# Kernel optimization log

Measured on AMD Instinct MI355X. Metric: run time of the kernel, lower is better.

## Reference

```python
import jax, jax.numpy as jnp
import numpy as np

D_MODEL = 2048
NUM_HEADS = 32
NUM_KV_HEADS = 8
DIM_HEAD = D_MODEL // NUM_HEADS  # 64
REPS = NUM_HEADS // NUM_KV_HEADS  # 4
B, T = 2, 2048


def setup_inputs() -> dict:
    key = jax.random.key(0)
    k_x, k_q, k_k, k_v, k_o = jax.random.split(key, 5)
    s = 1.0 / np.sqrt(D_MODEL)
    return {
        "x": jax.random.normal(k_x, (B, T, D_MODEL), dtype=jnp.float32),
        "wq": jax.random.normal(k_q, (D_MODEL, NUM_HEADS * DIM_HEAD), dtype=jnp.float32) * s,
        "wk": jax.random.normal(k_k, (D_MODEL, NUM_KV_HEADS * DIM_HEAD), dtype=jnp.float32) * s,
        "wv": jax.random.normal(k_v, (D_MODEL, NUM_KV_HEADS * DIM_HEAD), dtype=jnp.float32) * s,
        "wo": jax.random.normal(k_o, (D_MODEL, D_MODEL), dtype=jnp.float32) * s,
    }


def reference(x, wq, wk, wv, wo):
    Bb, Tt, _ = x.shape
    q = (x @ wq).reshape(Bb, Tt, NUM_HEADS, DIM_HEAD)       # [B,T,H,dh]
    k = (x @ wk).reshape(Bb, Tt, NUM_KV_HEADS, DIM_HEAD)    # [B,T,Hkv,dh]
    v = (x @ wv).reshape(Bb, Tt, NUM_KV_HEADS, DIM_HEAD)
    # repeat_interleave KV heads to match Q heads
    k = jnp.repeat(k, REPS, axis=2)                          # [B,T,H,dh]
    v = jnp.repeat(v, REPS, axis=2)
    scale = 1.0 / np.sqrt(DIM_HEAD).astype(np.float32)
    scores = jnp.einsum('bqhd,bkhd->bhqk', q, k) * scale     # [B,H,T,T]
    causal = jnp.tril(jnp.ones((Tt, Tt), dtype=bool))
    scores = jnp.where(causal, scores, -jnp.inf)
    attn = jax.nn.softmax(scores, axis=-1)
    out = jnp.einsum('bhqk,bkhd->bqhd', attn, v)             # [B,T,H,dh]
    out = out.reshape(Bb, Tt, NUM_HEADS * DIM_HEAD)
    return out @ wo
```

## Files before the change

### kernel.cpp

```cpp
#include <hip/hip_runtime.h>

typedef unsigned short u16;
typedef unsigned int u32;
typedef unsigned long long u64;

typedef __bf16 bf16x8 __attribute__((ext_vector_type(8)));
typedef float f32x4 __attribute__((ext_vector_type(4)));
typedef u16 u16x4 __attribute__((ext_vector_type(4)));

__device__ __forceinline__ u16 f2bf(float f) {
  u32 u = __builtin_bit_cast(u32, f);
  u += 0x7fffu + ((u >> 16) & 1u);
  return (u16)(u >> 16);
}

__device__ __forceinline__ u32 packbf2(float a, float b) {
  __bf16 x = (__bf16)a, y = (__bf16)b;
  return (u32)__builtin_bit_cast(u16, x) | ((u32)__builtin_bit_cast(u16, y) << 16);
}

__device__ __forceinline__ float fexp2(float x) {
#if __has_builtin(__builtin_amdgcn_exp2f)
  return __builtin_amdgcn_exp2f(x);
#else
  return exp2f(x);
#endif
}

__device__ __forceinline__ void gload_lds16(const void* g, void* lds) {
  __builtin_amdgcn_global_load_lds(
      (const __attribute__((address_space(1))) void*)g,
      (__attribute__((address_space(3))) void*)lds, 16, 0, 0);
}

#define QSCALE 0.18033688011112043f

__global__ __launch_bounds__(256) void prep_kernel(
    const float* __restrict__ x, u16* __restrict__ xb,
    const float* __restrict__ wq, const float* __restrict__ wk,
    const float* __restrict__ wv, const float* __restrict__ wo,
    u16* __restrict__ wqT, u16* __restrict__ wkT,
    u16* __restrict__ wvT, u16* __restrict__ woT) {
  __shared__ float tile[32][33];
  int bid = blockIdx.x;
  if (bid < 8192) {
    int i = (bid * 256 + threadIdx.x) * 4;
    float4 v = *reinterpret_cast<const float4*>(x + i);
    u16x4 o;
    o[0] = f2bf(v.x); o[1] = f2bf(v.y); o[2] = f2bf(v.z); o[3] = f2bf(v.w);
    *reinterpret_cast<u16x4*>(xb + i) = o;
    return;
  }
  bid -= 8192;
  constexpr int K = 2048;
  const float* w_;
  u16* wt;
  int N;
  switch (bid >> 12) {
    case 0: w_ = wq; wt = wqT; N = 2048; break;
    case 1: w_ = wo; wt = woT; N = 2048; break;
    case 2: w_ = wk; wt = wkT; N = 512; break;
    default: w_ = wv; wt = wvT; N = 512; break;
  }
  int rem = bid & 4095;
  int bx = (rem & 63) * 32;
  if (bx >= N) return;
  int by = (rem >> 6) * 32;
  int tx = threadIdx.x & 31, ty = threadIdx.x >> 5;
#pragma unroll
  for (int i = 0; i < 32; i += 8)
    tile[ty + i][tx] = w_[(size_t)(by + ty + i) * N + bx + tx];
  __syncthreads();
#pragma unroll
  for (int i = 0; i < 32; i += 8)
    wt[(size_t)(bx + ty + i) * K + by + tx] = f2bf(tile[tx][ty + i]);
}

__global__ __launch_bounds__(512, 1) void gemm_qkv(
    const u16* __restrict__ A, const u16* __restrict__ BT,
    u16* __restrict__ Cb, u16* __restrict__ Cb2, u16* __restrict__ Cb3) {
  constexpr int K = 2048, NT = 32;
  __shared__ __align__(16) u16 Ab[2][256 * 64];
  __shared__ __align__(16) u16 Bb[2][192 * 64];
  const int t = threadIdx.x;
  const int lane = t & 63;
  const int w = t >> 6;
  const int wm = w >> 2, wn = w & 3;
  const int l15 = lane & 15, l4 = lane >> 4;

  const int nwg = gridDim.x * gridDim.y;
  const int bid = blockIdx.y * gridDim.x + blockIdx.x;
  const int wg = (bid & 7) * (nwg >> 3) + (bid >> 3);
  const int brow = (wg / gridDim.x) * 256;
  const int bcol = (wg % gridDim.x) * 192;

  const int r0 = t >> 3;
  const int gc = ((t & 7) ^ (r0 & 7)) * 8;
  auto stageA = [&](int q, int h, int kt) {
    const u16* src = A + (size_t)(brow + h * 128 + r0) * K + kt * 64 + gc;
    u16* dst = &Ab[q][(h * 128 + r0) * 64 + (t & 7) * 8];
    gload_lds16(src, dst);
    gload_lds16(src + (size_t)64 * K, dst + 64 * 64);
  };
  auto stageB = [&](int q, int c, int kt) {
    const u16* src = BT + (size_t)(bcol + c * 64 + r0) * K + kt * 64 + gc;
    u16* dst = &Bb[q][(c * 64 + r0) * 64 + (t & 7) * 8];
    gload_lds16(src, dst);
  };

  f32x4 acc[8][3];
#pragma unroll
  for (int mi = 0; mi < 8; mi++)
#pragma unroll
    for (int n = 0; n < 3; n++)
#pragma unroll
      for (int r = 0; r < 4; r++) acc[mi][n][r] = 0.f;

  stageA(0, 0, 0); stageA(0, 1, 0);
  stageB(0, 0, 0); stageB(0, 1, 0); stageB(0, 2, 0);
  stageA(1, 0, 1); stageA(1, 1, 1);
  asm volatile("s_waitcnt vmcnt(4)" ::: "memory");
  __builtin_amdgcn_sched_barrier(0);
  __builtin_amdgcn_s_barrier();

  for (int kt = 0; kt < NT; ++kt) {
    const int q = kt & 1;
    const u16* Al = Ab[q];
    const u16* Bl = Bb[q];
    bf16x8 af[8][2], bf[3][2];

#pragma unroll
    for (int m = 0; m < 4; ++m) {
      int row = wm * 128 + m * 16 + l15;
#pragma unroll
      for (int ks = 0; ks < 2; ++ks)
        af[m][ks] = *reinterpret_cast<const bf16x8*>(
            &Al[row * 64 + (((ks * 4 + l4) ^ (row & 7)) * 8)]);
    }
#pragma unroll
    for (int n = 0; n < 3; ++n) {
      int row = wn * 48 + n * 16 + l15;
#pragma unroll
      for (int ks = 0; ks < 2; ++ks)
        bf[n][ks] = *reinterpret_cast<const bf16x8*>(
            &Bl[row * 64 + (((ks * 4 + l4) ^ (row & 7)) * 8)]);
    }
    if (kt + 1 < NT) stageB(q ^ 1, 0, kt + 1);
    __builtin_amdgcn_s_barrier();
    __builtin_amdgcn_s_setprio(1);
#pragma unroll
    for (int ks = 0; ks < 2; ++ks)
#pragma unroll
      for (int m = 0; m < 4; ++m)
#pragma unroll
        for (int n = 0; n < 2; ++n)
          acc[m][n] = __builtin_amdgcn_mfma_f32_16x16x32_bf16(
              af[m][ks], bf[n][ks], acc[m][n], 0, 0, 0);
    __builtin_amdgcn_s_setprio(0);
    __builtin_amdgcn_s_barrier();

#pragma unroll
    for (int m = 4; m < 8; ++m) {
      int row = wm * 128 + m * 16 + l15;
#pragma unroll
      for (int ks = 0; ks < 2; ++ks)
        af[m][ks] = *reinterpret_cast<const bf16x8*>(
            &Al[row * 64 + (((ks * 4 + l4) ^ (row & 7)) * 8)]);
    }
    if (kt + 1 < NT) { stageB(q ^ 1, 1, kt + 1); stageB(q ^ 1, 2, kt + 1); }
    __builtin_amdgcn_s_barrier();
    __builtin_amdgcn_s_setprio(1);
#pragma unroll
    for (int ks = 0; ks < 2; ++ks)
#pragma unroll
      for (int m = 0; m < 4; ++m)
        acc[m][2] = __builtin_amdgcn_mfma_f32_16x16x32_bf16(
            af[m][ks], bf[2][ks], acc[m][2], 0, 0, 0);
    __builtin_amdgcn_s_setprio(0);
    __builtin_amdgcn_s_barrier();

    if (kt + 2 < NT) stageA(q, 0, kt + 2);
    __builtin_amdgcn_s_barrier();
    __builtin_amdgcn_s_setprio(1);
#pragma unroll
    for (int ks = 0; ks < 2; ++ks)
#pragma unroll
      for (int m = 4; m < 8; ++m)
#pragma unroll
        for (int n = 0; n < 2; ++n)
          acc[m][n] = __builtin_amdgcn_mfma_f32_16x16x32_bf16(
              af[m][ks], bf[n][ks], acc[m][n], 0, 0, 0);
    __builtin_amdgcn_s_setprio(0);
    __builtin_amdgcn_s_barrier();

    if (kt + 2 < NT) stageA(q, 1, kt + 2);
    __builtin_amdgcn_s_barrier();
    __builtin_amdgcn_s_setprio(1);
#pragma unroll
    for (int ks = 0; ks < 2; ++ks)
#pragma unroll
      for (int m = 4; m < 8; ++m)
        acc[m][2] = __builtin_amdgcn_mfma_f32_16x16x32_bf16(
            af[m][ks], bf[2][ks], acc[m][2], 0, 0, 0);
    __builtin_amdgcn_s_setprio(0);
    if (kt + 2 < NT) {
      asm volatile("s_waitcnt vmcnt(4)" ::: "memory");
    } else {
      asm volatile("s_waitcnt vmcnt(0)" ::: "memory");
    }
    __builtin_amdgcn_sched_barrier(0);
    __builtin_amdgcn_s_barrier();
  }

#pragma unroll
  for (int mi = 0; mi < 8; ++mi) {
    int grow0 = brow + wm * 128 + mi * 16 + l4 * 4;
#pragma unroll
    for (int n = 0; n < 3; ++n) {
      int gbase = bcol + wn * 48 + n * 16;
      int gcol = gbase + l15;
      if (gbase < 2048) {
#pragma unroll
        for (int r = 0; r < 4; ++r)
          Cb[(size_t)(grow0 + r) * 2048 + gcol] = f2bf(acc[mi][n][r] * QSCALE);
      } else if (gbase < 2560) {
#pragma unroll
        for (int r = 0; r < 4; ++r)
          Cb2[(size_t)(grow0 + r) * 512 + (gcol - 2048)] = f2bf(acc[mi][n][r]);
      } else {
        int col = gcol - 2560;
        int bb = grow0 >> 11, tt = grow0 & 2047;
        u64 wv = (u64)packbf2(acc[mi][n][0], acc[mi][n][1]) |
                 ((u64)packbf2(acc[mi][n][2], acc[mi][n][3]) << 32);
        *reinterpret_cast<u64*>(&Cb3[((size_t)(bb * 512 + col)) * 2048 + tt]) = wv;
      }
    }
  }
}

__global__ __launch_bounds__(512, 2) void gemm256n(
    const u16* __restrict__ A, const u16* __restrict__ BT,
    float* __restrict__ Cf, int M, int N) {
  constexpr int K = 2048, NT = 32;
  __shared__ __align__(16) u16 Ab[2][256 * 64];
  __shared__ __align__(16) u16 Bb[2][128 * 64];
  const int t = threadIdx.x;
  const int lane = t & 63;
  const int w = t >> 6;
  const int wm = w >> 1, wn = w & 1;
  const int l15 = lane & 15, l4 = lane >> 4;

  const int nwg = gridDim.x * gridDim.y;
  const int bid = blockIdx.y * gridDim.x + blockIdx.x;
  const int wg = (bid & 7) * (nwg >> 3) + (bid >> 3);
  const int brow = (wg / gridDim.x) * 256;
  const int bcol = (wg % gridDim.x) * 128;

  const int r0 = t >> 3;
  const int gc = ((t & 7) ^ (r0 & 7)) * 8;
  auto stageA = [&](int q, int h, int kt) {
    const u16* src = A + (size_t)(brow + h * 128 + r0) * K + kt * 64 + gc;
    u16* dst = &Ab[q][(h * 128 + r0) * 64 + (t & 7) * 8];
    gload_lds16(src, dst);
    gload_lds16(src + (size_t)64 * K, dst + 64 * 64);
  };
  auto stageB = [&](int q, int h, int kt) {
    const u16* src = BT + (size_t)(bcol + h * 64 + r0) * K + kt * 64 + gc;
    u16* dst = &Bb[q][(h * 64 + r0) * 64 + (t & 7) * 8];
    gload_lds16(src, dst);
  };

  f32x4 acc[4][4];
#pragma unroll
  for (int m = 0; m < 4; m++)
#pragma unroll
    for (int n = 0; n < 4; n++)
#pragma unroll
      for (int r = 0; r < 4; r++) acc[m][n][r] = 0.f;

  stageA(0, 0, 0); stageA(0, 1, 0);
  stageB(0, 0, 0); stageB(0, 1, 0);
  stageA(1, 0, 1); stageA(1, 1, 1);
  asm volatile("s_waitcnt vmcnt(4)" ::: "memory");
  __builtin_amdgcn_sched_barrier(0);
  __builtin_amdgcn_s_barrier();

  for (int kt = 0; kt < NT; ++kt) {
    const int q = kt & 1;
    const u16* Al = Ab[q];
    const u16* Bl = Bb[q];
    bf16x8 af[4][2], bf[4][2];

#pragma unroll
    for (int m = 0; m < 2; ++m) {
      int row = wm * 64 + m * 16 + l15;
#pragma unroll
      for (int ks = 0; ks < 2; ++ks)
        af[m][ks] = *reinterpret_cast<const bf16x8*>(
            &Al[row * 64 + (((ks * 4 + l4) ^ (row & 7)) * 8)]);
    }
#pragma unroll
    for (int n = 0; n < 2; ++n) {
      int row = wn * 64 + n * 16 + l15;
#pragma unroll
      for (int ks = 0; ks < 2; ++ks)
        bf[n][ks] = *reinterpret_cast<const bf16x8*>(
            &Bl[row * 64 + (((ks * 4 + l4) ^ (row & 7)) * 8)]);
    }
    if (kt + 1 < NT) stageB(q ^ 1, 0, kt + 1);
    __builtin_amdgcn_s_barrier();
    __builtin_amdgcn_s_setprio(1);
#pragma unroll
    for (int ks = 0; ks < 2; ++ks)
#pragma unroll
      for (int m = 0; m < 2; ++m)
#pragma unroll
        for (int n = 0; n < 2; ++n)
          acc[m][n] = __builtin_amdgcn_mfma_f32_16x16x32_bf16(
              af[m][ks], bf[n][ks], acc[m][n], 0, 0, 0);
    __builtin_amdgcn_s_setprio(0);
    __builtin_amdgcn_s_barrier();

#pragma unroll
    for (int m = 2; m < 4; ++m) {
      int row = wm * 64 + m * 16 + l15;
#pragma unroll
      for (int ks = 0; ks < 2; ++ks)
        af[m][ks] = *reinterpret_cast<const bf16x8*>(
            &Al[row * 64 + (((ks * 4 + l4) ^ (row & 7)) * 8)]);
    }
#pragma unroll
    for (int n = 2; n < 4; ++n) {
      int row = wn * 64 + n * 16 + l15;
#pragma unroll
      for (int ks = 0; ks < 2; ++ks)
        bf[n][ks] = *reinterpret_cast<const bf16x8*>(
            &Bl[row * 64 + (((ks * 4 + l4) ^ (row & 7)) * 8)]);
    }
    if (kt + 1 < NT) stageB(q ^ 1, 1, kt + 1);
    __builtin_amdgcn_s_barrier();
    __builtin_amdgcn_s_setprio(1);
#pragma unroll
    for (int ks = 0; ks < 2; ++ks)
#pragma unroll
      for (int m = 0; m < 2; ++m)
#pragma unroll
        for (int n = 2; n < 4; ++n)
          acc[m][n] = __builtin_amdgcn_mfma_f32_16x16x32_bf16(
              af[m][ks], bf[n][ks], acc[m][n], 0, 0, 0);
    __builtin_amdgcn_s_setprio(0);
    __builtin_amdgcn_s_barrier();

    if (kt + 2 < NT) stageA(q, 0, kt + 2);
    __builtin_amdgcn_s_barrier();
    __builtin_amdgcn_s_setprio(1);
#pragma unroll
    for (int ks = 0; ks < 2; ++ks)
#pragma unroll
      for (int m = 2; m < 4; ++m)
#pragma unroll
        for (int n = 0; n < 2; ++n)
          acc[m][n] = __builtin_amdgcn_mfma_f32_16x16x32_bf16(
              af[m][ks], bf[n][ks], acc[m][n], 0, 0, 0);
    __builtin_amdgcn_s_setprio(0);
    __builtin_amdgcn_s_barrier();

    if (kt + 2 < NT) stageA(q, 1, kt + 2);
    __builtin_amdgcn_s_barrier();
    __builtin_amdgcn_s_setprio(1);
#pragma unroll
    for (int ks = 0; ks < 2; ++ks)
#pragma unroll
      for (int m = 2; m < 4; ++m)
#pragma unroll
        for (int n = 2; n < 4; ++n)
          acc[m][n] = __builtin_amdgcn_mfma_f32_16x16x32_bf16(
              af[m][ks], bf[n][ks], acc[m][n], 0, 0, 0);
    __builtin_amdgcn_s_setprio(0);
    if (kt + 2 < NT) {
      asm volatile("s_waitcnt vmcnt(4)" ::: "memory");
    } else {
      asm volatile("s_waitcnt vmcnt(0)" ::: "memory");
    }
    __builtin_amdgcn_sched_barrier(0);
    __builtin_amdgcn_s_barrier();
  }

#pragma unroll
  for (int m = 0; m < 4; ++m) {
    int grow0 = brow + wm * 64 + m * 16 + l4 * 4;
#pragma unroll
    for (int n = 0; n < 4; ++n) {
      int gcol = bcol + wn * 64 + n * 16 + l15;
#pragma unroll
      for (int r = 0; r < 4; ++r)
        Cf[(size_t)(grow0 + r) * N + gcol] = acc[m][n][r];
    }
  }
}

__global__ __launch_bounds__(256, 4) void attn_kernel(
    const u16* __restrict__ Qb, const u16* __restrict__ Kb,
    const u16* __restrict__ VT, u16* __restrict__ Ob) {
  const int bx = blockIdx.x;
  const int kvh = bx & 7;
  const int u = bx >> 3;
  const int jj = u & 15;
  const int v = u >> 4;
  const int h = kvh * 4 + (v & 3);
  const int b = v >> 2;
  const int t = threadIdx.x;
  const int lane = t & 63;
  const int w = t >> 6;
  const int q15 = lane & 15, g = lane >> 4;

  __shared__ __align__(16) u16 Ks[2][64 * 64];
  __shared__ __align__(16) u16 Vs[2][64 * 64];
  __shared__ __align__(16) u32 Pu[4][16 * 32];

  const size_t Krow0 = (size_t)b * 2048;
  const size_t Vrow0 = ((size_t)b * 8 + kvh) * 64;

  u16* const dk0 = &Ks[0][t * 8];
  u16* const dk1 = &Ks[1][t * 8];
  u16* const dv0 = &Vs[0][t * 8];
  u16* const dv1 = &Vs[1][t * 8];
  const int row0 = t >> 3;
  const int gcs = ((t & 7) ^ (row0 & 7)) * 8;
  const u16* const pk0 = Kb + (Krow0 + row0) * 512 + kvh * 64 + gcs;
  const u16* const pv0 = VT + (Vrow0 + row0) * 2048 + gcs;
  const u16* kp = pk0;
  const u16* vp = pv0;

  auto stage = [&](int buf, const u16* kpp, const u16* vpp) {
    u16* dk = buf ? dk1 : dk0;
    u16* dv = buf ? dv1 : dv0;
    gload_lds16(kpp, dk);
    gload_lds16(kpp + 32 * 512, dk + 2048);
    gload_lds16(vpp, dv);
    gload_lds16(vpp + 32 * 2048, dv + 2048);
  };

  const int swzB = (q15 & 7) << 3;
  const int swzP = (q15 & 7) << 2;
  u32* const pw = &Pu[w][0];
  const int nA = 32 - jj;
  const int nsteps = 33;

  stage(0, kp, vp);
  __syncthreads();
  int cur = 0;
  int ss = 0;

#pragma unroll
  for (int ph = 0; ph < 2; ++ph) {
    const int qt = ph ? jj : 31 - jj;
    const int nkv = qt + 1;
    const int wq0 = qt * 64 + w * 16;

    bf16x8 qf[2];
    {
      const u16* q0 = &Qb[((size_t)b * 2048 + wq0 + q15) * 2048 + h * 64 + g * 8];
      qf[0] = *reinterpret_cast<const bf16x8*>(q0);
      qf[1] = *reinterpret_cast<const bf16x8*>(q0 + 32);
    }

    f32x4 oo[4];
#pragma unroll
    for (int c = 0; c < 4; c++)
#pragma unroll
      for (int r = 0; r < 4; r++) oo[c][r] = 0.f;
    float mr = -1e30f, lr = 0.f;

    for (int kv = 0; kv < nkv; ++kv, ++ss) {
      const int kvbase = kv << 6;
      if (ss + 1 < nsteps) {
        if (ss + 1 == nA) {
          kp = pk0;
          vp = pv0;
        } else {
          kp += 64 * 512;
          vp += 64;
        }
        stage(cur ^ 1, kp, vp);
      }

      f32x4 s[4];
#pragma unroll
      for (int c = 0; c < 4; c++)
#pragma unroll
        for (int r = 0; r < 4; r++) s[c][r] = 0.f;
      __builtin_amdgcn_s_setprio(1);
#pragma unroll
      for (int ks = 0; ks < 2; ++ks) {
        const int kcol = (ks * 32 + g * 8) ^ swzB;
#pragma unroll
        for (int c = 0; c < 4; c++) {
          bf16x8 kb = *reinterpret_cast<const bf16x8*>(
              &Ks[cur][(c * 16 + q15) * 64 + kcol]);
          s[c] = __builtin_amdgcn_mfma_f32_16x16x32_bf16(kb, qf[ks], s[c], 0, 0, 0);
        }
      }
      __builtin_amdgcn_s_setprio(0);

      if (kv == qt) {
        const int qg = wq0 + q15;
#pragma unroll
        for (int c = 0; c < 4; c++)
#pragma unroll
          for (int r = 0; r < 4; r++)
            if (kvbase + c * 16 + g * 4 + r > qg) s[c][r] = -1e30f;
      }

      float mx0 = fmaxf(fmaxf(s[0][0], s[0][1]), fmaxf(s[0][2], s[0][3]));
      float mx1 = fmaxf(fmaxf(s[1][0], s[1][1]), fmaxf(s[1][2], s[1][3]));
      float mx2 = fmaxf(fmaxf(s[2][0], s[2][1]), fmaxf(s[2][2], s[2][3]));
      float mx3 = fmaxf(fmaxf(s[3][0], s[3][1]), fmaxf(s[3][2], s[3][3]));
      float mx = fmaxf(fmaxf(mx0, mx1), fmaxf(mx2, mx3));
      mx = fmaxf(mx, __shfl_xor(mx, 16));
      mx = fmaxf(mx, __shfl_xor(mx, 32));
      if (!__all(mx <= mr + 8.f)) {
        float mnew = fmaxf(mr, mx);
        float alpha = fexp2(mr - mnew);
        lr *= alpha;
#pragma unroll
        for (int c = 0; c < 4; c++)
#pragma unroll
          for (int r = 0; r < 4; r++) oo[c][r] *= alpha;
        mr = mnew;
      }
      float p[4][4];
      float rs = 0.f;
#pragma unroll
      for (int c = 0; c < 4; c++) {
        float t0 = fexp2(s[c][0] - mr);
        float t1 = fexp2(s[c][1] - mr);
        float t2 = fexp2(s[c][2] - mr);
        float t3 = fexp2(s[c][3] - mr);
        p[c][0] = t0; p[c][1] = t1; p[c][2] = t2; p[c][3] = t3;
        rs += (t0 + t1) + (t2 + t3);
      }
      rs += __shfl_xor(rs, 16);
      rs += __shfl_xor(rs, 32);
      lr += rs;
#pragma unroll
      for (int c = 0; c < 4; c++) {
        u64 wv = (u64)packbf2(p[c][0], p[c][1]) |
                 ((u64)packbf2(p[c][2], p[c][3]) << 32);
        *reinterpret_cast<u64*>(&pw[q15 * 32 + ((c * 8 + g * 2) ^ swzP)]) = wv;
      }
      bf16x8 pb[2];
#pragma unroll
      for (int ks = 0; ks < 2; ++ks)
        pb[ks] = *reinterpret_cast<const bf16x8*>(
            &pw[q15 * 32 + ((ks * 16 + g * 4) ^ swzP)]);

      __builtin_amdgcn_s_setprio(1);
#pragma unroll
      for (int ks = 0; ks < 2; ++ks) {
        const int vcol = (ks * 32 + g * 8) ^ swzB;
#pragma unroll
        for (int c2 = 0; c2 < 4; c2++) {
          bf16x8 vb = *reinterpret_cast<const bf16x8*>(
              &Vs[cur][(c2 * 16 + q15) * 64 + vcol]);
          oo[c2] = __builtin_amdgcn_mfma_f32_16x16x32_bf16(vb, pb[ks], oo[c2], 0, 0, 0);
        }
      }
      __builtin_amdgcn_s_setprio(0);

      __syncthreads();
      cur ^= 1;
    }

    const int qq = lane >> 2, cl = lane & 3;
    const int swq = (qq & 7) << 2;
    {
      float rcp = 1.0f / lr;
#pragma unroll
      for (int c2 = 0; c2 < 4; c2++) {
        u64 wv = (u64)packbf2(oo[c2][0] * rcp, oo[c2][1] * rcp) |
                 ((u64)packbf2(oo[c2][2] * rcp, oo[c2][3] * rcp) << 32);
        *reinterpret_cast<u64*>(&pw[q15 * 32 + ((c2 * 8 + g * 2) ^ swzP)]) = wv;
      }
      uint4 d0 = *reinterpret_cast<const uint4*>(&pw[qq * 32 + ((cl * 4) ^ swq)]);
      uint4 d1 = *reinterpret_cast<const uint4*>(&pw[qq * 32 + ((cl * 4 + 16) ^ swq)]);
      u32* og = (u32*)Ob + ((size_t)b * 2048 + wq0 + qq) * 1024 + h * 32;
      *reinterpret_cast<uint4*>(&og[cl * 4]) = d0;
      *reinterpret_cast<uint4*>(&og[cl * 4 + 16]) = d1;
    }
  }
}

extern "C" void kernel_launch(void* const* d_in, const int* in_sizes, int n_in,
                              void* d_out, int out_size, void* d_ws, size_t ws_size,
                              hipStream_t stream) {
  const float* x = (const float*)d_in[0];
  const float* wq = (const float*)d_in[1];
  const float* wk = (const float*)d_in[2];
  const float* wv = (const float*)d_in[3];
  const float* wo = (const float*)d_in[4];
  float* out = (float*)d_out;

  char* p = (char*)d_ws;
  u16* xb = (u16*)p;   p += (size_t)4096 * 2048 * 2;
  u16* wqT = (u16*)p;  p += (size_t)2048 * 2048 * 2;
  u16* wkT = (u16*)p;  p += (size_t)512 * 2048 * 2;
  u16* wvT = (u16*)p;  p += (size_t)512 * 2048 * 2;
  u16* woT = (u16*)p;  p += (size_t)2048 * 2048 * 2;
  u16* Qb = (u16*)p;   p += (size_t)4096 * 2048 * 2;
  u16* Kb = (u16*)p;   p += (size_t)4096 * 512 * 2;
  u16* VTb = (u16*)p;  p += (size_t)2 * 512 * 2048 * 2;
  u16* attn = xb;

  prep_kernel<<<8192 + 16384, 256, 0, stream>>>(
      x, xb, wq, wk, wv, wo, wqT, wkT, wvT, woT);

  gemm_qkv<<<dim3(16, 16), 512, 0, stream>>>(xb, wqT, Qb, Kb, VTb);

  attn_kernel<<<1024, 256, 0, stream>>>(Qb, Kb, VTb, attn);

  gemm256n<<<dim3(2048 / 128, 4096 / 256), 512, 0, stream>>>(
      attn, woT, out, 4096, 2048);
}
```

Before: 185.1 us.

## Use 32x32 MFMA with 128-row query tiles in attention, keep P in registers

The attention kernel moves from 64-row to 128-row query tiles, with each wave owning 32 query rows. QK^T and PV now use 32x32x16 bf16 MFMAs, halving the grid to 512 blocks with launch bounds lowered to 2. The P matrix is rearranged between lanes with cross-half shuffles instead of an LDS round-trip, and waves skip KV tiles that lie wholly beyond their causal limit. This aims to reuse each staged K/V tile across more queries and cut LDS traffic, at the cost of more registers, lower occupancy, fewer blocks and some idle waves on diagonal tiles.

```diff
diff --git a/kernel.cpp b/kernel.cpp
--- a/kernel.cpp
+++ b/kernel.cpp
@@ -6,7 +6,9 @@
 
 typedef __bf16 bf16x8 __attribute__((ext_vector_type(8)));
 typedef float f32x4 __attribute__((ext_vector_type(4)));
+typedef float f32x16 __attribute__((ext_vector_type(16)));
 typedef u16 u16x4 __attribute__((ext_vector_type(4)));
+typedef u32 u32x4v __attribute__((ext_vector_type(4)));
 
 __device__ __forceinline__ u16 f2bf(float f) {
   u32 u = __builtin_bit_cast(u32, f);
@@ -399,24 +401,25 @@
   }
 }
 
-__global__ __launch_bounds__(256, 4) void attn_kernel(
+__global__ __launch_bounds__(256, 2) void attn_kernel(
     const u16* __restrict__ Qb, const u16* __restrict__ Kb,
     const u16* __restrict__ VT, u16* __restrict__ Ob) {
   const int bx = blockIdx.x;
   const int kvh = bx & 7;
   const int u = bx >> 3;
-  const int jj = u & 15;
-  const int v = u >> 4;
+  const int jj = u & 7;
+  const int v = u >> 3;
   const int h = kvh * 4 + (v & 3);
   const int b = v >> 2;
   const int t = threadIdx.x;
   const int lane = t & 63;
   const int w = t >> 6;
-  const int q15 = lane & 15, g = lane >> 4;
+  const int q31 = lane & 31;
+  const int hi = lane >> 5;
 
   __shared__ __align__(16) u16 Ks[2][64 * 64];
   __shared__ __align__(16) u16 Vs[2][64 * 64];
-  __shared__ __align__(16) u32 Pu[4][16 * 32];
+  __shared__ __align__(16) u32 Po[4][32 * 32];
 
   const size_t Krow0 = (size_t)b * 2048;
   const size_t Vrow0 = ((size_t)b * 8 + kvh) * 64;
@@ -441,11 +444,9 @@
     gload_lds16(vpp + 32 * 2048, dv + 2048);
   };
 
-  const int swzB = (q15 & 7) << 3;
-  const int swzP = (q15 & 7) << 2;
-  u32* const pw = &Pu[w][0];
-  const int nA = 32 - jj;
-  const int nsteps = 33;
+  const int swk = (q31 & 7);
+  const int nA = 2 * (15 - jj) + 2;
+  const int nsteps = 34;
 
   stage(0, kp, vp);
   __syncthreads();
@@ -454,22 +455,23 @@
 
 #pragma unroll
   for (int ph = 0; ph < 2; ++ph) {
-    const int qt = ph ? jj : 31 - jj;
-    const int nkv = qt + 1;
-    const int wq0 = qt * 64 + w * 16;
-
-    bf16x8 qf[2];
+    const int qt = ph ? jj : 15 - jj;
+    const int nkv = 2 * qt + 2;
+    const int wq0 = qt * 128 + w * 32;
+    const int mylast = (wq0 + 31) >> 6;
+
+    bf16x8 qf[4];
     {
-      const u16* q0 = &Qb[((size_t)b * 2048 + wq0 + q15) * 2048 + h * 64 + g * 8];
+      const u16* q0 = &Qb[((size_t)b * 2048 + wq0 + q31) * 2048 + h * 64 + hi * 8];
       qf[0] = *reinterpret_cast<const bf16x8*>(q0);
-      qf[1] = *reinterpret_cast<const bf16x8*>(q0 + 32);
-    }
-
-    f32x4 oo[4];
-#pragma unroll
-    for (int c = 0; c < 4; c++)
-#pragma unroll
-      for (int r = 0; r < 4; r++) oo[c][r] = 0.f;
+      qf[1] = *reinterpret_cast<const bf16x8*>(q0 + 16);
+      qf[2] = *reinterpret_cast<const bf16x8*>(q0 + 32);
+      qf[3] = *reinterpret_cast<const bf16x8*>(q0 + 48);
+    }
+
+    f32x16 oo0, oo1;
+#pragma unroll
+    for (int r = 0; r < 16; ++r) { oo0[r] = 0.f; oo1[r] = 0.f; }
     float mr = -1e30f, lr = 0.f;
 
     for (int kv = 0; kv < nkv; ++kv, ++ss) {
@@ -485,109 +487,138 @@
         stage(cur ^ 1, kp, vp);
       }
 
-      f32x4 s[4];
-#pragma unroll
-      for (int c = 0; c < 4; c++)
-#pragma unroll
-        for (int r = 0; r < 4; r++) s[c][r] = 0.f;
-      __builtin_amdgcn_s_setprio(1);
-#pragma unroll
-      for (int ks = 0; ks < 2; ++ks) {
-        const int kcol = (ks * 32 + g * 8) ^ swzB;
-#pragma unroll
-        for (int c = 0; c < 4; c++) {
-          bf16x8 kb = *reinterpret_cast<const bf16x8*>(
-              &Ks[cur][(c * 16 + q15) * 64 + kcol]);
-          s[c] = __builtin_amdgcn_mfma_f32_16x16x32_bf16(kb, qf[ks], s[c], 0, 0, 0);
+      if (kv <= mylast) {
+        f32x16 s0, s1;
+#pragma unroll
+        for (int r = 0; r < 16; ++r) { s0[r] = 0.f; s1[r] = 0.f; }
+        __builtin_amdgcn_s_setprio(1);
+#pragma unroll
+        for (int kc = 0; kc < 4; ++kc) {
+          const int kcol = ((kc * 2 + hi) ^ swk) * 8;
+          bf16x8 kb0 = *reinterpret_cast<const bf16x8*>(&Ks[cur][q31 * 64 + kcol]);
+          bf16x8 kb1 = *reinterpret_cast<const bf16x8*>(&Ks[cur][(32 + q31) * 64 + kcol]);
+          s0 = __builtin_amdgcn_mfma_f32_32x32x16_bf16(kb0, qf[kc], s0, 0, 0, 0);
+          s1 = __builtin_amdgcn_mfma_f32_32x32x16_bf16(kb1, qf[kc], s1, 0, 0, 0);
         }
+        __builtin_amdgcn_s_setprio(0);
+
+        if (kvbase + 63 > wq0) {
+          const int qg = wq0 + q31;
+#pragma unroll
+          for (int r = 0; r < 16; ++r) {
+            int crow = ((r >> 2) << 3) + (r & 3) + 4 * hi;
+            if (kvbase + crow > qg) s0[r] = -1e30f;
+            if (kvbase + 32 + crow > qg) s1[r] = -1e30f;
+          }
+        }
+
+        float mt[8];
+#pragma unroll
+        for (int r = 0; r < 8; ++r)
+          mt[r] = fmaxf(fmaxf(s0[r], s0[r + 8]), fmaxf(s1[r], s1[r + 8]));
+#pragma unroll
+        for (int st = 4; st; st >>= 1)
+#pragma unroll
+          for (int r = 0; r < 8; ++r)
+            if (r < st) mt[r] = fmaxf(mt[r], mt[r + st]);
+        float mx = fmaxf(mt[0], __shfl_xor(mt[0], 32));
+        if (!__all(mx <= mr + 8.f)) {
+          float mnew = fmaxf(mr, mx);
+          float alpha = fexp2(mr - mnew);
+          lr *= alpha;
+#pragma unroll
+          for (int r = 0; r < 16; ++r) { oo0[r] *= alpha; oo1[r] *= alpha; }
+          mr = mnew;
+        }
+        float st_[8];
+#pragma unroll
+        for (int r = 0; r < 16; ++r) {
+          s0[r] = fexp2(s0[r] - mr);
+          s1[r] = fexp2(s1[r] - mr);
+        }
+#pragma unroll
+        for (int r = 0; r < 8; ++r)
+          st_[r] = (s0[r] + s0[r + 8]) + (s1[r] + s1[r + 8]);
+#pragma unroll
+        for (int stp = 4; stp; stp >>= 1)
+#pragma unroll
+          for (int r = 0; r < 8; ++r)
+            if (r < stp) st_[r] += st_[r + stp];
+        float rs = st_[0] + __shfl_xor(st_[0], 32);
+        lr += rs;
+
+        u32 W0[4][2], W1[4][2];
+#pragma unroll
+        for (int rr = 0; rr < 4; ++rr)
+#pragma unroll
+          for (int sx = 0; sx < 2; ++sx) {
+            W0[rr][sx] = packbf2(s0[4 * rr + 2 * sx], s0[4 * rr + 2 * sx + 1]);
+            W1[rr][sx] = packbf2(s1[4 * rr + 2 * sx], s1[4 * rr + 2 * sx + 1]);
+          }
+        bf16x8 pb[4];
+#pragma unroll
+        for (int cc = 0; cc < 2; ++cc) {
+          const int rrA = 2 * cc, rrB = 2 * cc + 1;
+          {
+            u32 z0 = hi ? W0[rrA][0] : W0[rrB][0];
+            u32 z1 = hi ? W0[rrA][1] : W0[rrB][1];
+            u32 z0x = (u32)__shfl_xor((int)z0, 32);
+            u32 z1x = (u32)__shfl_xor((int)z1, 32);
+            u32x4v pv4 = {hi ? z0x : W0[rrA][0], hi ? z1x : W0[rrA][1],
+                          hi ? W0[rrB][0] : z0x, hi ? W0[rrB][1] : z1x};
+            pb[cc] = __builtin_bit_cast(bf16x8, pv4);
+          }
+          {
+            u32 z0 = hi ? W1[rrA][0] : W1[rrB][0];
+            u32 z1 = hi ? W1[rrA][1] : W1[rrB][1];
+            u32 z0x = (u32)__shfl_xor((int)z0, 32);
+            u32 z1x = (u32)__shfl_xor((int)z1, 32);
+            u32x4v pv4 = {hi ? z0x : W1[rrA][0], hi ? z1x : W1[rrA][1],
+                          hi ? W1[rrB][0] : z0x, hi ? W1[rrB][1] : z1x};
+            pb[2 + cc] = __builtin_bit_cast(bf16x8, pv4);
+          }
+        }
+
+        __builtin_amdgcn_s_setprio(1);
+#pragma unroll
+        for (int kc2 = 0; kc2 < 4; ++kc2) {
+          const int vcol = ((kc2 * 2 + hi) ^ swk) * 8;
+          bf16x8 va0 = *reinterpret_cast<const bf16x8*>(&Vs[cur][q31 * 64 + vcol]);
+          bf16x8 va1 = *reinterpret_cast<const bf16x8*>(&Vs[cur][(32 + q31) * 64 + vcol]);
+          oo0 = __builtin_amdgcn_mfma_f32_32x32x16_bf16(va0, pb[kc2], oo0, 0, 0, 0);
+          oo1 = __builtin_amdgcn_mfma_f32_32x32x16_bf16(va1, pb[kc2], oo1, 0, 0, 0);
+        }
+        __builtin_amdgcn_s_setprio(0);
       }
-      __builtin_amdgcn_s_setprio(0);
-
-      if (kv == qt) {
-        const int qg = wq0 + q15;
-#pragma unroll
-        for (int c = 0; c < 4; c++)
-#pragma unroll
-          for (int r = 0; r < 4; r++)
-            if (kvbase + c * 16 + g * 4 + r > qg) s[c][r] = -1e30f;
-      }
-
-      float mx0 = fmaxf(fmaxf(s[0][0], s[0][1]), fmaxf(s[0][2], s[0][3]));
-      float mx1 = fmaxf(fmaxf(s[1][0], s[1][1]), fmaxf(s[1][2], s[1][3]));
-      float mx2 = fmaxf(fmaxf(s[2][0], s[2][1]), fmaxf(s[2][2], s[2][3]));
-      float mx3 = fmaxf(fmaxf(s[3][0], s[3][1]), fmaxf(s[3][2], s[3][3]));
-      float mx = fmaxf(fmaxf(mx0, mx1), fmaxf(mx2, mx3));
-      mx = fmaxf(mx, __shfl_xor(mx, 16));
-      mx = fmaxf(mx, __shfl_xor(mx, 32));
-      if (!__all(mx <= mr + 8.f)) {
-        float mnew = fmaxf(mr, mx);
-        float alpha = fexp2(mr - mnew);
-        lr *= alpha;
-#pragma unroll
-        for (int c = 0; c < 4; c++)
-#pragma unroll
-          for (int r = 0; r < 4; r++) oo[c][r] *= alpha;
-        mr = mnew;
-      }
-      float p[4][4];
-      float rs = 0.f;
-#pragma unroll
-      for (int c = 0; c < 4; c++) {
-        float t0 = fexp2(s[c][0] - mr);
-        float t1 = fexp2(s[c][1] - mr);
-        float t2 = fexp2(s[c][2] - mr);
-        float t3 = fexp2(s[c][3] - mr);
-        p[c][0] = t0; p[c][1] = t1; p[c][2] = t2; p[c][3] = t3;
-        rs += (t0 + t1) + (t2 + t3);
-      }
-      rs += __shfl_xor(rs, 16);
-      rs += __shfl_xor(rs, 32);
-      lr += rs;
-#pragma unroll
-      for (int c = 0; c < 4; c++) {
-        u64 wv = (u64)packbf2(p[c][0], p[c][1]) |
-                 ((u64)packbf2(p[c][2], p[c][3]) << 32);
-        *reinterpret_cast<u64*>(&pw[q15 * 32 + ((c * 8 + g * 2) ^ swzP)]) = wv;
-      }
-      bf16x8 pb[2];
-#pragma unroll
-      for (int ks = 0; ks < 2; ++ks)
-        pb[ks] = *reinterpret_cast<const bf16x8*>(
-            &pw[q15 * 32 + ((ks * 16 + g * 4) ^ swzP)]);
-
-      __builtin_amdgcn_s_setprio(1);
-#pragma unroll
-      for (int ks = 0; ks < 2; ++ks) {
-        const int vcol = (ks * 32 + g * 8) ^ swzB;
-#pragma unroll
-        for (int c2 = 0; c2 < 4; c2++) {
-          bf16x8 vb = *reinterpret_cast<const bf16x8*>(
-              &Vs[cur][(c2 * 16 + q15) * 64 + vcol]);
-          oo[c2] = __builtin_amdgcn_mfma_f32_16x16x32_bf16(vb, pb[ks], oo[c2], 0, 0, 0);
-        }
-      }
-      __builtin_amdgcn_s_setprio(0);
 
       __syncthreads();
       cur ^= 1;
     }
 
-    const int qq = lane >> 2, cl = lane & 3;
-    const int swq = (qq & 7) << 2;
     {
       float rcp = 1.0f / lr;
-#pragma unroll
-      for (int c2 = 0; c2 < 4; c2++) {
-        u64 wv = (u64)packbf2(oo[c2][0] * rcp, oo[c2][1] * rcp) |
-                 ((u64)packbf2(oo[c2][2] * rcp, oo[c2][3] * rcp) << 32);
-        *reinterpret_cast<u64*>(&pw[q15 * 32 + ((c2 * 8 + g * 2) ^ swzP)]) = wv;
+      u32* po = &Po[w][0];
+      const int swq = (q31 & 7) << 2;
+#pragma unroll
+      for (int rr = 0; rr < 4; ++rr) {
+        u64 w0 = (u64)packbf2(oo0[4 * rr] * rcp, oo0[4 * rr + 1] * rcp) |
+                 ((u64)packbf2(oo0[4 * rr + 2] * rcp, oo0[4 * rr + 3] * rcp) << 32);
+        *reinterpret_cast<u64*>(&po[q31 * 32 + ((4 * rr + 2 * hi) ^ swq)]) = w0;
+        u64 w1 = (u64)packbf2(oo1[4 * rr] * rcp, oo1[4 * rr + 1] * rcp) |
+                 ((u64)packbf2(oo1[4 * rr + 2] * rcp, oo1[4 * rr + 3] * rcp) << 32);
+        *reinterpret_cast<u64*>(&po[q31 * 32 + ((16 + 4 * rr + 2 * hi) ^ swq)]) = w1;
       }
-      uint4 d0 = *reinterpret_cast<const uint4*>(&pw[qq * 32 + ((cl * 4) ^ swq)]);
-      uint4 d1 = *reinterpret_cast<const uint4*>(&pw[qq * 32 + ((cl * 4 + 16) ^ swq)]);
-      u32* og = (u32*)Ob + ((size_t)b * 2048 + wq0 + qq) * 1024 + h * 32;
-      *reinterpret_cast<uint4*>(&og[cl * 4]) = d0;
-      *reinterpret_cast<uint4*>(&og[cl * 4 + 16]) = d1;
-    }
+      const int qq = lane >> 1, hf = lane & 1;
+      const int swr = (qq & 7) << 2;
+      u32* og = (u32*)Ob + ((size_t)b * 2048 + wq0 + qq) * 1024 + h * 32 + hf * 16;
+#pragma unroll
+      for (int j = 0; j < 4; ++j) {
+        uint4 d = *reinterpret_cast<const uint4*>(
+            &po[qq * 32 + ((hf * 16 + j * 4) ^ swr)]);
+        *reinterpret_cast<uint4*>(&og[j * 4]) = d;
+      }
+    }
+    __syncthreads();
   }
 }
 
@@ -617,7 +648,7 @@
 
   gemm_qkv<<<dim3(16, 16), 512, 0, stream>>>(xb, wqT, Qb, Kb, VTb);
 
-  attn_kernel<<<1024, 256, 0, stream>>>(Qb, Kb, VTb, attn);
+  attn_kernel<<<512, 256, 0, stream>>>(Qb, Kb, VTb, attn);
 
   gemm256n<<<dim3(2048 / 128, 4096 / 256), 512, 0, stream>>>(
       attn, woT, out, 4096, 2048);
```

Result: no change. 184.2 us (-0.5%).
